# Kernel optimization log

Hardware: AMD Instinct MI355X
Metric: run time of the kernel (lower is better)

Reference implementation:

```python
import jax, jax.numpy as jnp
import numpy as np

N, E, D, H = 100000, 1600000, 128, 2  # nodes, edges, channels (in=out), heads
NEG_SLOPE = 0.2
EPS = 1e-16


def setup_inputs() -> dict:
    key = jax.random.key(0)
    ks = jax.random.split(key, 12)
    s = 1.0 / np.sqrt(D)
    return {
        "x": jax.random.normal(ks[0], (N, D), jnp.float32),
        "edge_index": jax.random.randint(ks[1], (2, E), 0, N, jnp.int64),
        "gamma": jnp.ones((D,), jnp.float32),
        "beta": jnp.zeros((D,), jnp.float32),
        "Wl": jax.random.normal(ks[2], (D, H * D), jnp.float32) * s,
        "bl": jnp.zeros((H * D,), jnp.float32),
        "Wr": jax.random.normal(ks[3], (D, H * D), jnp.float32) * s,
        "br": jnp.zeros((H * D,), jnp.float32),
        "att": jax.random.normal(ks[4], (H, D), jnp.float32) * s,
        "res_W": jax.random.normal(ks[5], (D, D), jnp.float32) * s,
        "bias": jnp.zeros((D,), jnp.float32),
    }


def _segment_softmax(alpha, seg, num_segments):
    m = jax.ops.segment_max(alpha, seg, num_segments=num_segments)
    a = jnp.exp(alpha - m[seg])
    z = jax.ops.segment_sum(a, seg, num_segments=num_segments)
    return a / (z[seg] + EPS)


def reference(x, edge_index, gamma, beta, Wl, bl, Wr, br, att, res_W, bias):
    n = x.shape[0]
    residual = x
    # per-node LayerNorm -> ReLU
    mu = x.mean(-1, keepdims=True)
    var = ((x - mu) ** 2).mean(-1, keepdims=True)
    h = (x - mu) * jax.lax.rsqrt(var + 1e-5) * gamma + beta
    h = jax.nn.relu(h)
    # GATv2: per-node linear transforms [N,H,D]
    xl = (h @ Wl + bl).reshape(n, H, D)  # source-side
    xr = (h @ Wr + br).reshape(n, H, D)  # target-side
    src, dst = edge_index[0], edge_index[1]
    e = jax.nn.leaky_relu(xl[src] + xr[dst], NEG_SLOPE)  # [E,H,D]
    alpha = jnp.einsum('ehd,hd->eh', e, att)             # [E,H]
    alpha = _segment_softmax(alpha, dst, n)
    msg = xl[src] * alpha[..., None]                     # [E,H,D]
    out = jax.ops.segment_sum(msg, dst, num_segments=n)  # [N,H,D]
    out = out.mean(axis=1)                               # concat=False -> mean heads
    out = out + h @ res_W + bias                         # GATv2 internal residual + bias
    return residual + out
```

## Files before the change

### kernel.cpp

```cpp
#include <hip/hip_runtime.h>
#include <hip/hip_bf16.h>
#include <cstdint>
#include <cstddef>

#define DCH 128
#define NHEADS 2
#define NEG_SLOPE 0.2f

typedef __attribute__((ext_vector_type(8))) short short8v;
typedef __attribute__((ext_vector_type(4))) float f32x4;
typedef __attribute__((ext_vector_type(2))) float f32x2;
typedef _Float16 h4 __attribute__((ext_vector_type(4)));

__device__ __forceinline__ unsigned short f2bf(float f) {
    union { float f; unsigned int i; } v; v.f = f;
    unsigned int r = v.i + 0x7fffu + ((v.i >> 16) & 1u);
    return (unsigned short)(r >> 16);
}
__device__ __forceinline__ unsigned short f2h_bits(float f) {
    _Float16 h = (_Float16)f;
    union { _Float16 h; unsigned short u; } v; v.h = h; return v.u;
}

__device__ __forceinline__ float halfsum(float p) {
    p += __int_as_float(__builtin_amdgcn_update_dpp(
            0, __float_as_int(p), 0x121, 0xF, 0xF, false));
    p += __int_as_float(__builtin_amdgcn_update_dpp(
            0, __float_as_int(p), 0x122, 0xF, 0xF, false));
    p += __int_as_float(__builtin_amdgcn_update_dpp(
            0, __float_as_int(p), 0x124, 0xF, 0xF, false));
    p += __int_as_float(__builtin_amdgcn_update_dpp(
            0, __float_as_int(p), 0x128, 0xF, 0xF, false));
    p += __int_as_float(__builtin_amdgcn_ds_swizzle(
            __float_as_int(p), 0x401F));
    return p;
}

__global__ void prep_and_zero(const float* __restrict__ Wl, const float* __restrict__ Wr,
                              const float* __restrict__ resW,
                              unsigned short* __restrict__ wfrag,
                              int* __restrict__ cnt, int n) {
    if (blockIdx.x >= 40) {
        int i = (blockIdx.x - 40) * 256 + threadIdx.x;
        if (i < n) cnt[i] = 0;
        return;
    }
    int gid  = blockIdx.x * 256 + threadIdx.x;
    int lane = gid & 63;
    int f    = gid >> 6;
    int ks   = f & 3;
    int ct   = f >> 2;
    int col  = ct * 16 + (lane & 15);
    int k0   = ks * 32 + (lane >> 4) * 8;
    const float* W; int ldB, c;
    if (col < 256)      { W = Wl;   ldB = 256; c = col; }
    else if (col < 512) { W = Wr;   ldB = 256; c = col - 256; }
    else                { W = resW; ldB = 128; c = col - 512; }
    unsigned short tmp[8];
#pragma unroll
    for (int j = 0; j < 8; ++j) tmp[j] = f2bf(W[(size_t)(k0 + j) * ldB + c]);
    ushort4* dst = (ushort4*)(wfrag + (size_t)gid * 8);
    dst[0] = make_ushort4(tmp[0], tmp[1], tmp[2], tmp[3]);
    dst[1] = make_ushort4(tmp[4], tmp[5], tmp[6], tmp[7]);
}

__launch_bounds__(256)
__global__ void gemm_fill(const float* __restrict__ x,
                          const float* __restrict__ gamma, const float* __restrict__ beta,
                          const unsigned short* __restrict__ wfrag,
                          const float* __restrict__ bl, const float* __restrict__ br,
                          const float* __restrict__ bias,
                          unsigned char* __restrict__ xl8, unsigned short* __restrict__ xr,
                          float* __restrict__ out, int n,
                          const int* __restrict__ srcIdx, const int* __restrict__ dstIdx,
                          int* __restrict__ fillc, int* __restrict__ sbuf, int E, int nrb) {
    __shared__ __align__(16) unsigned char smem[128 * 256];

    if ((int)blockIdx.x >= nrb) {
        int i = (blockIdx.x - nrb) * 256 + threadIdx.x;
        int E4 = E >> 2;
        if (i < E4) {
            int4 d = ((const int4*)dstIdx)[i];
            int4 s = ((const int4*)srcIdx)[i];
            sbuf[atomicAdd(&fillc[d.x], 1)] = s.x;
            sbuf[atomicAdd(&fillc[d.y], 1)] = s.y;
            sbuf[atomicAdd(&fillc[d.z], 1)] = s.z;
            sbuf[atomicAdd(&fillc[d.w], 1)] = s.w;
        }
        if (i < (E & 3)) {
            int e = E4 * 4 + i;
            sbuf[atomicAdd(&fillc[dstIdx[e]], 1)] = srcIdx[e];
        }
        return;
    }

    int row0 = blockIdx.x * 128;
    int tid  = threadIdx.x;
    unsigned short* As = (unsigned short*)smem;

    {
        int r  = tid >> 5;
        int k4 = (tid & 31) * 4;
        float4 g4  = *(const float4*)(gamma + k4);
        float4 be4 = *(const float4*)(beta + k4);
#pragma unroll
        for (int i = 0; i < 16; ++i) {
            int row  = r + i * 8;
            int grow = row0 + row;
            float4 a = (grow < n) ? *(const float4*)(x + (size_t)grow * DCH + k4)
                                  : make_float4(0.f, 0.f, 0.f, 0.f);
            float s  = a.x + a.y + a.z + a.w;
            float sq = a.x * a.x + a.y * a.y + a.z * a.z + a.w * a.w;
#pragma unroll
            for (int msk = 16; msk; msk >>= 1) {
                s  += __shfl_xor(s, msk);
                sq += __shfl_xor(sq, msk);
            }
            float mu = s * (1.f / DCH);
            float rs = rsqrtf(sq * (1.f / DCH) - mu * mu + 1e-5f);
            ushort4 u;
            u.x = f2bf(fmaxf((a.x - mu) * rs * g4.x + be4.x, 0.f));
            u.y = f2bf(fmaxf((a.y - mu) * rs * g4.y + be4.y, 0.f));
            u.z = f2bf(fmaxf((a.z - mu) * rs * g4.z + be4.z, 0.f));
            u.w = f2bf(fmaxf((a.w - mu) * rs * g4.w + be4.w, 0.f));
            int byteoff = row * 256 + ((k4 * 2) ^ ((row & 7) << 4));
            *(ushort4*)((char*)As + byteoff) = u;
        }
    }
    __syncthreads();

    int wv = tid >> 6, lane = tid & 63;

    short8v afrag[2][4];
#pragma unroll
    for (int g = 0; g < 2; ++g) {
        int arow = wv * 32 + g * 16 + (lane & 15);
#pragma unroll
        for (int ks = 0; ks < 4; ++ks) {
            int kbyte = (ks * 64 + (lane >> 4) * 16) ^ ((arow & 7) << 4);
            afrag[g][ks] = *(const short8v*)((const char*)As + arow * 256 + kbyte);
        }
    }
    __syncthreads();

    int nodeL0 = wv * 32 + (lane & 15);
    int nodeL1 = nodeL0 + 16;
    int cq = (lane >> 4) << 2;

    auto mfma_ct = [&](int ct, f32x4& a0, f32x4& a1) {
        const unsigned short* bp = wfrag + ((size_t)(ct * 4) * 64 + lane) * 8;
        short8v b0 = *(const short8v*)(bp);
        short8v b1 = *(const short8v*)(bp + 64 * 8);
        short8v b2 = *(const short8v*)(bp + 128 * 8);
        short8v b3 = *(const short8v*)(bp + 192 * 8);
        a0 = __builtin_amdgcn_mfma_f32_16x16x32_bf16(b0, afrag[0][0], a0, 0, 0, 0);
        a1 = __builtin_amdgcn_mfma_f32_16x16x32_bf16(b0, afrag[1][0], a1, 0, 0, 0);
        a0 = __builtin_amdgcn_mfma_f32_16x16x32_bf16(b1, afrag[0][1], a0, 0, 0, 0);
        a1 = __builtin_amdgcn_mfma_f32_16x16x32_bf16(b1, afrag[1][1], a1, 0, 0, 0);
        a0 = __builtin_amdgcn_mfma_f32_16x16x32_bf16(b2, afrag[0][2], a0, 0, 0, 0);
        a1 = __builtin_amdgcn_mfma_f32_16x16x32_bf16(b2, afrag[1][2], a1, 0, 0, 0);
        a0 = __builtin_amdgcn_mfma_f32_16x16x32_bf16(b3, afrag[0][3], a0, 0, 0, 0);
        a1 = __builtin_amdgcn_mfma_f32_16x16x32_bf16(b3, afrag[1][3], a1, 0, 0, 0);
    };

    {
#pragma unroll
        for (int ct = 0; ct < 16; ++ct) {
            f32x4 acc0 = {0.f, 0.f, 0.f, 0.f};
            f32x4 acc1 = {0.f, 0.f, 0.f, 0.f};
            mfma_ct(ct, acc0, acc1);
            int c = ct * 16 + cq;
            float4 bb = *(const float4*)(bl + c);
            int cb = ct * 16 + cq;
            int p0 = __builtin_amdgcn_cvt_pk_fp8_f32(acc0[0] + bb.x, acc0[1] + bb.y, 0, false);
            p0     = __builtin_amdgcn_cvt_pk_fp8_f32(acc0[2] + bb.z, acc0[3] + bb.w, p0, true);
            *(int*)(smem + nodeL0 * 256 + (cb ^ ((nodeL0 & 7) << 4))) = p0;
            int p1 = __builtin_amdgcn_cvt_pk_fp8_f32(acc1[0] + bb.x, acc1[1] + bb.y, 0, false);
            p1     = __builtin_amdgcn_cvt_pk_fp8_f32(acc1[2] + bb.z, acc1[3] + bb.w, p1, true);
            *(int*)(smem + nodeL1 * 256 + (cb ^ ((nodeL1 & 7) << 4))) = p1;
        }
        __syncthreads();
#pragma unroll
        for (int it = 0; it < 8; ++it) {
            int chunk = it * 256 + tid;
            int row  = chunk >> 4;
            int colb = (chunk & 15) * 16;
            int grow = row0 + row;
            if (grow < n) {
                int4 v = *(const int4*)(smem + row * 256 + (colb ^ ((row & 7) << 4)));
                *(int4*)(xl8 + (size_t)grow * 256 + colb) = v;
            }
        }
        __syncthreads();
    }

    for (int fg = 0; fg < 2; ++fg) {
#pragma unroll
        for (int ctl = 0; ctl < 8; ++ctl) {
            int ct = 16 + fg * 8 + ctl;
            f32x4 acc0 = {0.f, 0.f, 0.f, 0.f};
            f32x4 acc1 = {0.f, 0.f, 0.f, 0.f};
            mfma_ct(ct, acc0, acc1);
            int c = ct * 16 + cq - 256;
            float4 bb = *(const float4*)(br + c);
            int cb = ctl * 32 + cq * 2;
            ushort4 u0 = make_ushort4(f2h_bits(acc0[0] + bb.x), f2h_bits(acc0[1] + bb.y),
                                      f2h_bits(acc0[2] + bb.z), f2h_bits(acc0[3] + bb.w));
            *(ushort4*)(smem + nodeL0 * 256 + (cb ^ ((nodeL0 & 7) << 4))) = u0;
            ushort4 u1 = make_ushort4(f2h_bits(acc1[0] + bb.x), f2h_bits(acc1[1] + bb.y),
                                      f2h_bits(acc1[2] + bb.z), f2h_bits(acc1[3] + bb.w));
            *(ushort4*)(smem + nodeL1 * 256 + (cb ^ ((nodeL1 & 7) << 4))) = u1;
        }
        __syncthreads();
#pragma unroll
        for (int it = 0; it < 8; ++it) {
            int chunk = it * 256 + tid;
            int row  = chunk >> 4;
            int colb = (chunk & 15) * 16;
            int grow = row0 + row;
            if (grow < n) {
                int4 v = *(const int4*)(smem + row * 256 + (colb ^ ((row & 7) << 4)));
                *(int4*)((char*)xr + (size_t)grow * 512 + fg * 256 + colb) = v;
            }
        }
        __syncthreads();
    }

    for (int fg = 0; fg < 2; ++fg) {
#pragma unroll
        for (int ctl = 0; ctl < 4; ++ctl) {
            int ct = 32 + fg * 4 + ctl;
            f32x4 acc0 = {0.f, 0.f, 0.f, 0.f};
            f32x4 acc1 = {0.f, 0.f, 0.f, 0.f};
            mfma_ct(ct, acc0, acc1);
            int c = ct * 16 + cq - 512;
            float4 bb = *(const float4*)(bias + c);
            int cb = ctl * 64 + cq * 4;
            float4 w0 = make_float4(acc0[0] + bb.x, acc0[1] + bb.y,
                                    acc0[2] + bb.z, acc0[3] + bb.w);
            *(float4*)(smem + nodeL0 * 256 + (cb ^ ((nodeL0 & 7) << 4))) = w0;
            float4 w1 = make_float4(acc1[0] + bb.x, acc1[1] + bb.y,
                                    acc1[2] + bb.z, acc1[3] + bb.w);
            *(float4*)(smem + nodeL1 * 256 + (cb ^ ((nodeL1 & 7) << 4))) = w1;
        }
        __syncthreads();
#pragma unroll
        for (int it = 0; it < 8; ++it) {
            int chunk = it * 256 + tid;
            int row  = chunk >> 4;
            int colb = (chunk & 15) * 16;
            int grow = row0 + row;
            if (grow < n) {
                float4 v = *(const float4*)(smem + row * 256 + (colb ^ ((row & 7) << 4)));
                float4 xv = *(const float4*)((const char*)x + (size_t)grow * 512 + fg * 256 + colb);
                v.x += xv.x; v.y += xv.y; v.z += xv.z; v.w += xv.w;
                *(float4*)((char*)out + (size_t)grow * 512 + fg * 256 + colb) = v;
            }
        }
        __syncthreads();
    }
}

__global__ void hist_dst(const int* __restrict__ dst, int* __restrict__ cnt, int E) {
    int i = blockIdx.x * blockDim.x + threadIdx.x;
    int E4 = E >> 2;
    if (i < E4) {
        int4 d = ((const int4*)dst)[i];
        atomicAdd(&cnt[d.x], 1); atomicAdd(&cnt[d.y], 1);
        atomicAdd(&cnt[d.z], 1); atomicAdd(&cnt[d.w], 1);
    }
    if (i < (E & 3)) atomicAdd(&cnt[dst[E4 * 4 + i]], 1);
}

__global__ void scan_block(const int* __restrict__ cnt, int* __restrict__ offs,
                           int* __restrict__ bsum, int n) {
    __shared__ int sm[256];
    int t = threadIdx.x;
    int i = blockIdx.x * 256 + t;
    int v = (i < n) ? cnt[i] : 0;
    sm[t] = v;
    __syncthreads();
#pragma unroll
    for (int d = 1; d < 256; d <<= 1) {
        int add = (t >= d) ? sm[t - d] : 0;
        __syncthreads();
        sm[t] += add;
        __syncthreads();
    }
    if (i < n) offs[i] = sm[t] - v;
    if (t == 255) bsum[blockIdx.x] = sm[t];
}

__global__ void scan_bsum_par(int* __restrict__ bsum, int nb) {
    __shared__ int sm[512];
    int t = threadIdx.x;
    if (nb <= 512) {
        int v = (t < nb) ? bsum[t] : 0;
        sm[t] = v;
        __syncthreads();
#pragma unroll
        for (int d = 1; d < 512; d <<= 1) {
            int add = (t >= d) ? sm[t - d] : 0;
            __syncthreads();
            sm[t] += add;
            __syncthreads();
        }
        if (t < nb) bsum[t] = sm[t] - v;
    } else if (t == 0) {
        int acc = 0;
        for (int i = 0; i < nb; ++i) { int v = bsum[i]; bsum[i] = acc; acc += v; }
    }
}

__global__ void scan_add(int* __restrict__ offs, int* __restrict__ fillc,
                         const int* __restrict__ bsum, int n, int E) {
    int i = blockIdx.x * 256 + threadIdx.x;
    if (i < n) {
        int v = offs[i] + bsum[blockIdx.x];
        offs[i]  = v;
        fillc[i] = v;
    }
    if (i == 0) offs[n] = E;
}

__launch_bounds__(256)
__global__ void gat_aggregate(const int* __restrict__ offs, const int* __restrict__ sbuf,
                              const unsigned char* __restrict__ xl8,
                              const unsigned short* __restrict__ xr_,
                              const float* __restrict__ att,
                              float* __restrict__ out, int n) {
    const _Float16* xr = (const _Float16*)xr_;
    int lane = threadIdx.x & 63;
    int wid  = __builtin_amdgcn_readfirstlane((blockIdx.x * blockDim.x + threadIdx.x) >> 6);
    int nw   = (gridDim.x * blockDim.x) >> 6;

    const float LOG2E = 1.4426950408889634f;
    float4 af = *(const float4*)(att + lane * 4);
    float ax = af.x * LOG2E, ay = af.y * LOG2E, az = af.z * LOG2E, aw = af.w * LOG2E;

    for (int t = wid; t < n; t += nw) {
        int beg = offs[t];
        int end = offs[t + 1];
        if (beg == end) continue;
        h4 rr = *(const h4*)(xr + (size_t)t * 256 + lane * 4);
        float rx = (float)rr[0], ry = (float)rr[1], rz = (float)rr[2], rw = (float)rr[3];

        float m = -INFINITY, z = 0.f;
        float4 acc = make_float4(0.f, 0.f, 0.f, 0.f);

        auto process4 = [&](int u0, int u1, int u2, int u3) {
            f32x2 l0a = __builtin_amdgcn_cvt_pk_f32_fp8(u0, false);
            f32x2 l0b = __builtin_amdgcn_cvt_pk_f32_fp8(u0, true);
            f32x2 l1a = __builtin_amdgcn_cvt_pk_f32_fp8(u1, false);
            f32x2 l1b = __builtin_amdgcn_cvt_pk_f32_fp8(u1, true);
            f32x2 l2a = __builtin_amdgcn_cvt_pk_f32_fp8(u2, false);
            f32x2 l2b = __builtin_amdgcn_cvt_pk_f32_fp8(u2, true);
            f32x2 l3a = __builtin_amdgcn_cvt_pk_f32_fp8(u3, false);
            f32x2 l3b = __builtin_amdgcn_cvt_pk_f32_fp8(u3, true);

            auto logit = [&](f32x2 la, f32x2 lb) {
                float vx = la.x + rx; vx = fmaxf(vx, NEG_SLOPE * vx);
                float vy = la.y + ry; vy = fmaxf(vy, NEG_SLOPE * vy);
                float vz = lb.x + rz; vz = fmaxf(vz, NEG_SLOPE * vz);
                float vw = lb.y + rw; vw = fmaxf(vw, NEG_SLOPE * vw);
                return fmaf(vw, aw, fmaf(vz, az, fmaf(vy, ay, vx * ax)));
            };
            float p0 = halfsum(logit(l0a, l0b));
            float p1 = halfsum(logit(l1a, l1b));
            float p2 = halfsum(logit(l2a, l2b));
            float p3 = halfsum(logit(l3a, l3b));
            float pm = fmaxf(fmaxf(p0, p1), fmaxf(p2, p3));
            if (__any(pm - m > 11.5f)) {
                float mn = fmaxf(m, pm);
                float sc = __builtin_amdgcn_exp2f(m - mn);
                z *= sc;
                acc.x *= sc; acc.y *= sc; acc.z *= sc; acc.w *= sc;
                m = mn;
            }
            float w0 = __builtin_amdgcn_exp2f(p0 - m);
            float w1 = __builtin_amdgcn_exp2f(p1 - m);
            float w2 = __builtin_amdgcn_exp2f(p2 - m);
            float w3 = __builtin_amdgcn_exp2f(p3 - m);
            z += (w0 + w1) + (w2 + w3);
            acc.x = fmaf(l0a.x, w0, acc.x); acc.y = fmaf(l0a.y, w0, acc.y);
            acc.z = fmaf(l0b.x, w0, acc.z); acc.w = fmaf(l0b.y, w0, acc.w);
            acc.x = fmaf(l1a.x, w1, acc.x); acc.y = fmaf(l1a.y, w1, acc.y);
            acc.z = fmaf(l1b.x, w1, acc.z); acc.w = fmaf(l1b.y, w1, acc.w);
            acc.x = fmaf(l2a.x, w2, acc.x); acc.y = fmaf(l2a.y, w2, acc.y);
            acc.z = fmaf(l2b.x, w2, acc.z); acc.w = fmaf(l2b.y, w2, acc.w);
            acc.x = fmaf(l3a.x, w3, acc.x); acc.y = fmaf(l3a.y, w3, acc.y);
            acc.z = fmaf(l3b.x, w3, acc.z); acc.w = fmaf(l3b.y, w3, acc.w);
        };

        int j = beg;
        int c0, c1, c2, c3;
        bool have = (j + 4 <= end);
        if (have) {
            int s0 = sbuf[j], s1 = sbuf[j + 1], s2 = sbuf[j + 2], s3 = sbuf[j + 3];
            c0 = *(const int*)(xl8 + (size_t)s0 * 256 + lane * 4);
            c1 = *(const int*)(xl8 + (size_t)s1 * 256 + lane * 4);
            c2 = *(const int*)(xl8 + (size_t)s2 * 256 + lane * 4);
            c3 = *(const int*)(xl8 + (size_t)s3 * 256 + lane * 4);
        }
        for (; j + 8 <= end; j += 4) {
            int s0 = sbuf[j + 4], s1 = sbuf[j + 5], s2 = sbuf[j + 6], s3 = sbuf[j + 7];
            int n0 = *(const int*)(xl8 + (size_t)s0 * 256 + lane * 4);
            int n1 = *(const int*)(xl8 + (size_t)s1 * 256 + lane * 4);
            int n2 = *(const int*)(xl8 + (size_t)s2 * 256 + lane * 4);
            int n3 = *(const int*)(xl8 + (size_t)s3 * 256 + lane * 4);
            process4(c0, c1, c2, c3);
            c0 = n0; c1 = n1; c2 = n2; c3 = n3;
        }
        if (have) { process4(c0, c1, c2, c3); j += 4; }
        for (; j < end; ++j) {
            int u = *(const int*)(xl8 + (size_t)sbuf[j] * 256 + lane * 4);
            f32x2 la = __builtin_amdgcn_cvt_pk_f32_fp8(u, false);
            f32x2 lb = __builtin_amdgcn_cvt_pk_f32_fp8(u, true);
            float vx = la.x + rx; vx = fmaxf(vx, NEG_SLOPE * vx);
            float vy = la.y + ry; vy = fmaxf(vy, NEG_SLOPE * vy);
            float vz = lb.x + rz; vz = fmaxf(vz, NEG_SLOPE * vz);
            float vw = lb.y + rw; vw = fmaxf(vw, NEG_SLOPE * vw);
            float p = halfsum(fmaf(vw, aw, fmaf(vz, az, fmaf(vy, ay, vx * ax))));
            if (__any(p - m > 11.5f)) {
                float mn = fmaxf(m, p);
                float sc = __builtin_amdgcn_exp2f(m - mn);
                z *= sc;
                acc.x *= sc; acc.y *= sc; acc.z *= sc; acc.w *= sc;
                m = mn;
            }
            float w = __builtin_amdgcn_exp2f(p - m);
            z += w;
            acc.x = fmaf(la.x, w, acc.x); acc.y = fmaf(la.y, w, acc.y);
            acc.z = fmaf(lb.x, w, acc.z); acc.w = fmaf(lb.y, w, acc.w);
        }
        float inv = 0.5f / (z + 1e-16f);
        acc.x *= inv; acc.y *= inv; acc.z *= inv; acc.w *= inv;
        acc.x += __shfl_xor(acc.x, 32);
        acc.y += __shfl_xor(acc.y, 32);
        acc.z += __shfl_xor(acc.z, 32);
        acc.w += __shfl_xor(acc.w, 32);
        if (lane < 32) {
            float4* o = (float4*)(out + (size_t)t * DCH + lane * 4);
            float4 cur = *o;
            cur.x += acc.x; cur.y += acc.y; cur.z += acc.z; cur.w += acc.w;
            *o = cur;
        }
    }
}

extern "C" void kernel_launch(void* const* d_in, const int* in_sizes, int n_in,
                              void* d_out, int out_size, void* d_ws, size_t ws_size,
                              hipStream_t stream) {
    const float* x     = (const float*)d_in[0];
    const int*   ei    = (const int*)d_in[1];
    const float* gamma = (const float*)d_in[2];
    const float* beta  = (const float*)d_in[3];
    const float* Wl    = (const float*)d_in[4];
    const float* bl    = (const float*)d_in[5];
    const float* Wr    = (const float*)d_in[6];
    const float* br    = (const float*)d_in[7];
    const float* att   = (const float*)d_in[8];
    const float* resW  = (const float*)d_in[9];
    const float* bias  = (const float*)d_in[10];
    float* out = (float*)d_out;

    int n = in_sizes[0] / DCH;
    int E = in_sizes[1] / 2;
    const int* src = ei;
    const int* dstIdx = ei + E;

    char* ws = (char*)d_ws;
    size_t off = 0;
    auto alloc = [&](size_t bytes) -> void* {
        void* p = ws + off;
        off = (off + bytes + 255) & ~(size_t)255;
        return p;
    };

    int nb = (n + 255) / 256;

    unsigned char*  xl8 = (unsigned char*)alloc((size_t)n * 256);
    unsigned short* xr  = (unsigned short*)alloc((size_t)n * 256 * 2);
    unsigned short* wfrag = (unsigned short*)alloc(160 * 64 * 8 * 2);
    int* cnt   = (int*)alloc((size_t)n * 4);
    int* offs  = (int*)alloc((size_t)(n + 1) * 4);
    int* bsum  = (int*)alloc((size_t)nb * 4);
    int* fillc = (int*)alloc((size_t)n * 4);
    int* sbuf  = (int*)alloc((size_t)E * 4);

    prep_and_zero<<<40 + nb, 256, 0, stream>>>(Wl, Wr, resW, wfrag, cnt, n);
    int ethr = (E / 4 + 255) / 256 + 1;
    hist_dst<<<ethr, 256, 0, stream>>>(dstIdx, cnt, E);
    scan_block<<<nb, 256, 0, stream>>>(cnt, offs, bsum, n);
    scan_bsum_par<<<1, 512, 0, stream>>>(bsum, nb);
    scan_add<<<nb, 256, 0, stream>>>(offs, fillc, bsum, n, E);

    int nrb = (n + 127) / 128;
    gemm_fill<<<nrb + ethr, 256, 0, stream>>>(x, gamma, beta, wfrag, bl, br, bias,
                                              xl8, xr, out, n,
                                              src, dstIdx, fillc, sbuf, E, nrb);
    gat_aggregate<<<2048, 256, 0, stream>>>(offs, sbuf, xl8, xr, att, out, n);
}
```

Baseline: 292.8 us.

## Halve GEMM row tile to 64 and use one edge per thread in scatter

The fused LayerNorm+GEMM kernel now handles 64 rows per block instead of 128, so each wave computes one 16-row MFMA tile and LDS use is halved. This gives more blocks, higher occupancy and lower register pressure, but the weight fragments are reloaded twice as often per row. The histogram and CSR-fill paths move from four edges per thread with int4 loads to one edge per thread, spreading the atomics over more threads at the cost of more threads and scalar loads.

```diff
diff --git a/kernel.cpp b/kernel.cpp
--- a/kernel.cpp
+++ b/kernel.cpp
@@ -74,27 +74,19 @@
                           float* __restrict__ out, int n,
                           const int* __restrict__ srcIdx, const int* __restrict__ dstIdx,
                           int* __restrict__ fillc, int* __restrict__ sbuf, int E, int nrb) {
-    __shared__ __align__(16) unsigned char smem[128 * 256];
+    __shared__ __align__(16) unsigned char smem[64 * 256];
 
     if ((int)blockIdx.x >= nrb) {
         int i = (blockIdx.x - nrb) * 256 + threadIdx.x;
-        int E4 = E >> 2;
-        if (i < E4) {
-            int4 d = ((const int4*)dstIdx)[i];
-            int4 s = ((const int4*)srcIdx)[i];
-            sbuf[atomicAdd(&fillc[d.x], 1)] = s.x;
-            sbuf[atomicAdd(&fillc[d.y], 1)] = s.y;
-            sbuf[atomicAdd(&fillc[d.z], 1)] = s.z;
-            sbuf[atomicAdd(&fillc[d.w], 1)] = s.w;
-        }
-        if (i < (E & 3)) {
-            int e = E4 * 4 + i;
-            sbuf[atomicAdd(&fillc[dstIdx[e]], 1)] = srcIdx[e];
+        if (i < E) {
+            int d = dstIdx[i];
+            int s = srcIdx[i];
+            sbuf[atomicAdd(&fillc[d], 1)] = s;
         }
         return;
     }
 
-    int row0 = blockIdx.x * 128;
+    int row0 = blockIdx.x * 64;
     int tid  = threadIdx.x;
     unsigned short* As = (unsigned short*)smem;
 
@@ -104,7 +96,7 @@
         float4 g4  = *(const float4*)(gamma + k4);
         float4 be4 = *(const float4*)(beta + k4);
 #pragma unroll
-        for (int i = 0; i < 16; ++i) {
+        for (int i = 0; i < 8; ++i) {
             int row  = r + i * 8;
             int grow = row0 + row;
             float4 a = (grow < n) ? *(const float4*)(x + (size_t)grow * DCH + k4)
@@ -131,57 +123,47 @@
 
     int wv = tid >> 6, lane = tid & 63;
 
-    short8v afrag[2][4];
-#pragma unroll
-    for (int g = 0; g < 2; ++g) {
-        int arow = wv * 32 + g * 16 + (lane & 15);
+    short8v afrag[4];
+    {
+        int arow = wv * 16 + (lane & 15);
 #pragma unroll
         for (int ks = 0; ks < 4; ++ks) {
             int kbyte = (ks * 64 + (lane >> 4) * 16) ^ ((arow & 7) << 4);
-            afrag[g][ks] = *(const short8v*)((const char*)As + arow * 256 + kbyte);
+            afrag[ks] = *(const short8v*)((const char*)As + arow * 256 + kbyte);
         }
     }
     __syncthreads();
 
-    int nodeL0 = wv * 32 + (lane & 15);
-    int nodeL1 = nodeL0 + 16;
+    int nodeL = wv * 16 + (lane & 15);
     int cq = (lane >> 4) << 2;
 
-    auto mfma_ct = [&](int ct, f32x4& a0, f32x4& a1) {
+    auto mfma_ct = [&](int ct, f32x4& a0) {
         const unsigned short* bp = wfrag + ((size_t)(ct * 4) * 64 + lane) * 8;
         short8v b0 = *(const short8v*)(bp);
         short8v b1 = *(const short8v*)(bp + 64 * 8);
         short8v b2 = *(const short8v*)(bp + 128 * 8);
         short8v b3 = *(const short8v*)(bp + 192 * 8);
-        a0 = __builtin_amdgcn_mfma_f32_16x16x32_bf16(b0, afrag[0][0], a0, 0, 0, 0);
-        a1 = __builtin_amdgcn_mfma_f32_16x16x32_bf16(b0, afrag[1][0], a1, 0, 0, 0);
-        a0 = __builtin_amdgcn_mfma_f32_16x16x32_bf16(b1, afrag[0][1], a0, 0, 0, 0);
-        a1 = __builtin_amdgcn_mfma_f32_16x16x32_bf16(b1, afrag[1][1], a1, 0, 0, 0);
-        a0 = __builtin_amdgcn_mfma_f32_16x16x32_bf16(b2, afrag[0][2], a0, 0, 0, 0);
-        a1 = __builtin_amdgcn_mfma_f32_16x16x32_bf16(b2, afrag[1][2], a1, 0, 0, 0);
-        a0 = __builtin_amdgcn_mfma_f32_16x16x32_bf16(b3, afrag[0][3], a0, 0, 0, 0);
-        a1 = __builtin_amdgcn_mfma_f32_16x16x32_bf16(b3, afrag[1][3], a1, 0, 0, 0);
+        a0 = __builtin_amdgcn_mfma_f32_16x16x32_bf16(b0, afrag[0], a0, 0, 0, 0);
+        a0 = __builtin_amdgcn_mfma_f32_16x16x32_bf16(b1, afrag[1], a0, 0, 0, 0);
+        a0 = __builtin_amdgcn_mfma_f32_16x16x32_bf16(b2, afrag[2], a0, 0, 0, 0);
+        a0 = __builtin_amdgcn_mfma_f32_16x16x32_bf16(b3, afrag[3], a0, 0, 0, 0);
     };
 
     {
 #pragma unroll
         for (int ct = 0; ct < 16; ++ct) {
-            f32x4 acc0 = {0.f, 0.f, 0.f, 0.f};
-            f32x4 acc1 = {0.f, 0.f, 0.f, 0.f};
-            mfma_ct(ct, acc0, acc1);
+            f32x4 acc = {0.f, 0.f, 0.f, 0.f};
+            mfma_ct(ct, acc);
             int c = ct * 16 + cq;
             float4 bb = *(const float4*)(bl + c);
             int cb = ct * 16 + cq;
-            int p0 = __builtin_amdgcn_cvt_pk_fp8_f32(acc0[0] + bb.x, acc0[1] + bb.y, 0, false);
-            p0     = __builtin_amdgcn_cvt_pk_fp8_f32(acc0[2] + bb.z, acc0[3] + bb.w, p0, true);
-            *(int*)(smem + nodeL0 * 256 + (cb ^ ((nodeL0 & 7) << 4))) = p0;
-            int p1 = __builtin_amdgcn_cvt_pk_fp8_f32(acc1[0] + bb.x, acc1[1] + bb.y, 0, false);
-            p1     = __builtin_amdgcn_cvt_pk_fp8_f32(acc1[2] + bb.z, acc1[3] + bb.w, p1, true);
-            *(int*)(smem + nodeL1 * 256 + (cb ^ ((nodeL1 & 7) << 4))) = p1;
-        }
-        __syncthreads();
-#pragma unroll
-        for (int it = 0; it < 8; ++it) {
+            int p0 = __builtin_amdgcn_cvt_pk_fp8_f32(acc[0] + bb.x, acc[1] + bb.y, 0, false);
+            p0     = __builtin_amdgcn_cvt_pk_fp8_f32(acc[2] + bb.z, acc[3] + bb.w, p0, true);
+            *(int*)(smem + nodeL * 256 + (cb ^ ((nodeL & 7) << 4))) = p0;
+        }
+        __syncthreads();
+#pragma unroll
+        for (int it = 0; it < 4; ++it) {
             int chunk = it * 256 + tid;
             int row  = chunk >> 4;
             int colb = (chunk & 15) * 16;
@@ -198,22 +180,18 @@
 #pragma unroll
         for (int ctl = 0; ctl < 8; ++ctl) {
             int ct = 16 + fg * 8 + ctl;
-            f32x4 acc0 = {0.f, 0.f, 0.f, 0.f};
-            f32x4 acc1 = {0.f, 0.f, 0.f, 0.f};
-            mfma_ct(ct, acc0, acc1);
+            f32x4 acc = {0.f, 0.f, 0.f, 0.f};
+            mfma_ct(ct, acc);
             int c = ct * 16 + cq - 256;
             float4 bb = *(const float4*)(br + c);
             int cb = ctl * 32 + cq * 2;
-            ushort4 u0 = make_ushort4(f2h_bits(acc0[0] + bb.x), f2h_bits(acc0[1] + bb.y),
-                                      f2h_bits(acc0[2] + bb.z), f2h_bits(acc0[3] + bb.w));
-            *(ushort4*)(smem + nodeL0 * 256 + (cb ^ ((nodeL0 & 7) << 4))) = u0;
-            ushort4 u1 = make_ushort4(f2h_bits(acc1[0] + bb.x), f2h_bits(acc1[1] + bb.y),
-                                      f2h_bits(acc1[2] + bb.z), f2h_bits(acc1[3] + bb.w));
-            *(ushort4*)(smem + nodeL1 * 256 + (cb ^ ((nodeL1 & 7) << 4))) = u1;
-        }
-        __syncthreads();
-#pragma unroll
-        for (int it = 0; it < 8; ++it) {
+            ushort4 u = make_ushort4(f2h_bits(acc[0] + bb.x), f2h_bits(acc[1] + bb.y),
+                                     f2h_bits(acc[2] + bb.z), f2h_bits(acc[3] + bb.w));
+            *(ushort4*)(smem + nodeL * 256 + (cb ^ ((nodeL & 7) << 4))) = u;
+        }
+        __syncthreads();
+#pragma unroll
+        for (int it = 0; it < 4; ++it) {
             int chunk = it * 256 + tid;
             int row  = chunk >> 4;
             int colb = (chunk & 15) * 16;
@@ -230,22 +208,18 @@
 #pragma unroll
         for (int ctl = 0; ctl < 4; ++ctl) {
             int ct = 32 + fg * 4 + ctl;
-            f32x4 acc0 = {0.f, 0.f, 0.f, 0.f};
-            f32x4 acc1 = {0.f, 0.f, 0.f, 0.f};
-            mfma_ct(ct, acc0, acc1);
+            f32x4 acc = {0.f, 0.f, 0.f, 0.f};
+            mfma_ct(ct, acc);
             int c = ct * 16 + cq - 512;
             float4 bb = *(const float4*)(bias + c);
             int cb = ctl * 64 + cq * 4;
-            float4 w0 = make_float4(acc0[0] + bb.x, acc0[1] + bb.y,
-                                    acc0[2] + bb.z, acc0[3] + bb.w);
-            *(float4*)(smem + nodeL0 * 256 + (cb ^ ((nodeL0 & 7) << 4))) = w0;
-            float4 w1 = make_float4(acc1[0] + bb.x, acc1[1] + bb.y,
-                                    acc1[2] + bb.z, acc1[3] + bb.w);
-            *(float4*)(smem + nodeL1 * 256 + (cb ^ ((nodeL1 & 7) << 4))) = w1;
-        }
-        __syncthreads();
-#pragma unroll
-        for (int it = 0; it < 8; ++it) {
+            float4 w0 = make_float4(acc[0] + bb.x, acc[1] + bb.y,
+                                    acc[2] + bb.z, acc[3] + bb.w);
+            *(float4*)(smem + nodeL * 256 + (cb ^ ((nodeL & 7) << 4))) = w0;
+        }
+        __syncthreads();
+#pragma unroll
+        for (int it = 0; it < 4; ++it) {
             int chunk = it * 256 + tid;
             int row  = chunk >> 4;
             int colb = (chunk & 15) * 16;
@@ -263,13 +237,7 @@
 
 __global__ void hist_dst(const int* __restrict__ dst, int* __restrict__ cnt, int E) {
     int i = blockIdx.x * blockDim.x + threadIdx.x;
-    int E4 = E >> 2;
-    if (i < E4) {
-        int4 d = ((const int4*)dst)[i];
-        atomicAdd(&cnt[d.x], 1); atomicAdd(&cnt[d.y], 1);
-        atomicAdd(&cnt[d.z], 1); atomicAdd(&cnt[d.w], 1);
-    }
-    if (i < (E & 3)) atomicAdd(&cnt[dst[E4 * 4 + i]], 1);
+    if (i < E) atomicAdd(&cnt[dst[i]], 1);
 }
 
 __global__ void scan_block(const int* __restrict__ cnt, int* __restrict__ offs,
@@ -489,13 +457,13 @@
     int* sbuf  = (int*)alloc((size_t)E * 4);
 
     prep_and_zero<<<40 + nb, 256, 0, stream>>>(Wl, Wr, resW, wfrag, cnt, n);
-    int ethr = (E / 4 + 255) / 256 + 1;
+    int ethr = (E + 255) / 256;
     hist_dst<<<ethr, 256, 0, stream>>>(dstIdx, cnt, E);
     scan_block<<<nb, 256, 0, stream>>>(cnt, offs, bsum, n);
     scan_bsum_par<<<1, 512, 0, stream>>>(bsum, nb);
     scan_add<<<nb, 256, 0, stream>>>(offs, fillc, bsum, n, E);
 
-    int nrb = (n + 127) / 128;
+    int nrb = (n + 63) / 64;
     gemm_fill<<<nrb + ethr, 256, 0, stream>>>(x, gamma, beta, wfrag, bl, br, bias,
                                               xl8, xr, out, n,
                                               src, dstIdx, fillc, sbuf, E, nrb);
```

Result: slower. 357.2 us (+22.0%).
